# Optimization experiments

Hardware: AMD Instinct MI355X
Metric: run time of the kernel (lower is better)

Reference implementation:

```python
import jax, jax.numpy as jnp
import numpy as np

B, S, E = 2, 2048, 1024
H = 16
HD = E // H           # 64
KD = 64               # k_dim
VD = 64               # v_dim
SCALE = 1.0 / np.float32(np.sqrt(KD))


def setup_inputs() -> dict:
    key = jax.random.key(0)
    ks = jax.random.split(key, 10)
    return {
        "x": jax.random.normal(ks[0], (B, S, E), dtype=jnp.float32),
        "mask": jax.random.uniform(ks[1], (S, S), dtype=jnp.float32),
        "Wq": jax.random.normal(ks[2], (HD, KD), dtype=jnp.float32) * 0.05,
        "bq": jax.random.normal(ks[3], (KD,), dtype=jnp.float32) * 0.05,
        "Wk": jax.random.normal(ks[4], (HD, KD), dtype=jnp.float32) * 0.05,
        "bk": jax.random.normal(ks[5], (KD,), dtype=jnp.float32) * 0.05,
        "Wv": jax.random.normal(ks[6], (HD, VD), dtype=jnp.float32) * 0.05,
        "bv": jax.random.normal(ks[7], (VD,), dtype=jnp.float32) * 0.05,
        "Wo": jax.random.normal(ks[8], (H * VD, E), dtype=jnp.float32) * 0.05,
        "bo": jax.random.normal(ks[9], (E,), dtype=jnp.float32) * 0.05,
    }


def reference(x, mask, Wq, bq, Wk, bk, Wv, bv, Wo, bo):
    b, s, e = x.shape
    # (B, S, E) -> (B, H, S, head_dim)
    xh = x.reshape(b, s, H, HD).transpose(0, 2, 1, 3)
    q = jnp.einsum('bhsd,dk->bhsk', xh, Wq) + bq   # (B,H,S,KD)
    k = jnp.einsum('bhsd,dk->bhsk', xh, Wk) + bk   # (B,H,S,KD)
    v = jnp.einsum('bhsd,dv->bhsv', xh, Wv) + bv   # (B,H,S,VD)
    sim = jnp.einsum('bhqk,bhsk->bhqs', q, k) * SCALE  # (B,H,S,S)
    sim = sim * mask[None, None, :, :]                  # multiplicative mask
    attn = jax.nn.softmax(sim, axis=-1)
    out = jnp.einsum('bhqs,bhsv->bhqv', attn, v)        # (B,H,S,VD)
    out = out.transpose(0, 2, 1, 3).reshape(b, s, H * VD)
    return out @ Wo + bo
```

## Files before the change

### kernel.cpp

```cpp
#include <hip/hip_runtime.h>
#include <hip/hip_bf16.h>

#define SS 2048
#define EE 1024
#define SCALE 0.125f
#define LOG2E 1.44269504088896f

typedef __attribute__((ext_vector_type(8))) short short8;
typedef __attribute__((ext_vector_type(4))) float float4v;
typedef __attribute__((ext_vector_type(8))) unsigned short ushort8;

__device__ __forceinline__ float bf2f(unsigned short u) {
  unsigned int v = ((unsigned int)u) << 16;
  return __uint_as_float(v);
}
__device__ __forceinline__ unsigned short f2bf(float f) {
  unsigned int u = __float_as_uint(f);
  unsigned int lsb = (u >> 16) & 1u;
  u += 0x7fffu + lsb;
  return (unsigned short)(u >> 16);
}
__device__ __forceinline__ unsigned int pk2bf(float a, float b) {
  __hip_bfloat162 h = __float22bfloat162_rn(float2{a, b});
  return *reinterpret_cast<unsigned int*>(&h);
}

__global__ __launch_bounds__(256) void w3t_prep(
    const float* __restrict__ Wq, const float* __restrict__ Wk,
    const float* __restrict__ Wv, unsigned short* __restrict__ W3T)
{
  __shared__ unsigned short t[64 * 65];
  const float* W = (blockIdx.x == 0) ? Wq : (blockIdx.x == 1 ? Wk : Wv);
  int tid = threadIdx.x;
#pragma unroll
  for (int i = 0; i < 16; ++i) {
    int e = tid + i * 256; int d = e >> 6, n = e & 63;
    t[n * 65 + d] = f2bf(W[e]);
  }
  __syncthreads();
  unsigned short* dst = W3T + blockIdx.x * 4096;
#pragma unroll
  for (int i = 0; i < 16; ++i) {
    int e = tid + i * 256; int n = e >> 6, d = e & 63;
    dst[n * 64 + d] = t[n * 65 + d];
  }
}

__global__ __launch_bounds__(256) void qkv_kernel(
    const float* __restrict__ x, const unsigned short* __restrict__ W3T,
    const float* __restrict__ bq, const float* __restrict__ bk,
    const float* __restrict__ bv,
    unsigned short* __restrict__ Q, unsigned short* __restrict__ K,
    unsigned short* __restrict__ Vp)
{
  __shared__ __align__(16) unsigned short w3t[192 * 72];
  __shared__ __align__(16) unsigned short xt[64 * 72];
  __shared__ float sBias[192];
  int tid = threadIdx.x;
  int bh = blockIdx.x >> 5;
  int s0blk = (blockIdx.x & 31) * 64;
  int b = bh >> 4, h = bh & 15;

#pragma unroll
  for (int i = 0; i < 6; ++i) {
    int slot = tid + i * 256;
    int row = slot >> 3, c = slot & 7;
    *(short8*)(w3t + row * 72 + c * 8) = *(const short8*)(W3T + slot * 8);
  }
  if (tid < 192) sBias[tid] = (tid < 64) ? bq[tid] : (tid < 128 ? bk[tid - 64] : bv[tid - 128]);

  const float* xbase = x + ((size_t)(b * SS + s0blk)) * EE + h * 64;
#pragma unroll
  for (int it = 0; it < 4; ++it) {
    int flat = tid + it * 256;
    int row = flat >> 4, ch = flat & 15;
    float4 v = *(const float4*)(xbase + (size_t)row * EE + ch * 4);
    uint2 u; u.x = pk2bf(v.x, v.y); u.y = pk2bf(v.z, v.w);
    *(uint2*)(xt + row * 72 + ch * 4) = u;
  }
  __syncthreads();

  int wv = tid >> 6, lane = tid & 63;
  int li = lane & 15, g = lane >> 4;
  int mrow = wv * 16;

  short8 af[2];
#pragma unroll
  for (int ks = 0; ks < 2; ++ks)
    af[ks] = *(const short8*)(xt + (mrow + li) * 72 + ks * 32 + g * 8);

  float4v acc[12];
#pragma unroll
  for (int i = 0; i < 12; ++i) acc[i] = (float4v){0, 0, 0, 0};
#pragma unroll
  for (int ks = 0; ks < 2; ++ks)
#pragma unroll
    for (int nb = 0; nb < 12; ++nb) {
      short8 bfr = *(const short8*)(w3t + (nb * 16 + li) * 72 + ks * 32 + g * 8);
      acc[nb] = __builtin_amdgcn_mfma_f32_16x16x32_bf16(af[ks], bfr, acc[nb], 0, 0, 0);
    }

  int srow0 = s0blk + mrow + g * 4;
#pragma unroll
  for (int nb = 0; nb < 12; ++nb) {
    float bias = sBias[nb * 16 + li];
    int mtx = nb >> 2, sub = nb & 3;
#pragma unroll
    for (int r = 0; r < 4; ++r) {
      unsigned short ob = f2bf(acc[nb][r] + bias);
      int s = srow0 + r;
      if (mtx == 0)      Q[((size_t)bh * SS + s) * 64 + sub * 16 + li] = ob;
      else if (mtx == 1) K[((size_t)bh * SS + s) * 64 + sub * 16 + li] = ob;
      else {
        int sl = s & 31;
        int pos = ((sl & 15) << 1) | (sl >> 4);
        Vp[(size_t)bh * 131072 + (size_t)(s >> 5) * 2048 + (sub * 16 + li) * 32 + pos] = ob;
      }
    }
  }
}

__global__ __launch_bounds__(256) void mask_prep(
    const float* __restrict__ mask, unsigned short* __restrict__ maskP)
{
  int idx = blockIdx.x * 256 + threadIdx.x;
  int lane = idx & 63, t = (idx >> 6) & 63, qt = idx >> 12;
  int li = lane & 15, g = lane >> 4;
  const float c = SCALE * LOG2E;
  ushort8 o;
#pragma unroll
  for (int sb = 0; sb < 2; ++sb)
#pragma unroll
    for (int r = 0; r < 4; ++r)
      o[sb * 4 + r] = f2bf(mask[(size_t)(qt * 16 + g * 4 + r) * SS + t * 32 + sb * 16 + li] * c);
  *(ushort8*)(maskP + (size_t)idx * 8) = o;
}

__global__ __launch_bounds__(256) void attn_kernel(
    const unsigned short* __restrict__ Q, const unsigned short* __restrict__ K,
    const unsigned short* __restrict__ Vp, const unsigned short* __restrict__ maskP,
    unsigned short* __restrict__ AO)
{
  __shared__ __align__(16) unsigned short kt[32 * 88];
  __shared__ __align__(16) unsigned short vt[64 * 40];
  __shared__ __align__(16) unsigned short pt[4][2][16 * 40];

  int tid = threadIdx.x, wv = tid >> 6, lane = tid & 63;
  int li = lane & 15, g = lane >> 4;
  int bh = blockIdx.x >> 4;
  int q0 = (blockIdx.x & 15) * 128 + wv * 32;

  const unsigned short* Qb0 = Q + ((size_t)bh * SS + q0 + li) * 64;
  const unsigned short* Qb1 = Q + ((size_t)bh * SS + q0 + 16 + li) * 64;
  short8 qf[2][2];
  qf[0][0] = *(const short8*)(Qb0 + g * 8);
  qf[0][1] = *(const short8*)(Qb0 + 32 + g * 8);
  qf[1][0] = *(const short8*)(Qb1 + g * 8);
  qf[1][1] = *(const short8*)(Qb1 + 32 + g * 8);

  const unsigned short* Kg = K + (size_t)bh * SS * 64 + tid * 8;
  const unsigned short* Vg = Vp + (size_t)bh * 131072 + tid * 8;
  const unsigned short* Mg0 = maskP + (size_t)(q0 >> 4) * 32768 + lane * 8;
  const unsigned short* Mg1 = Mg0 + 32768;

  int kldso = (tid >> 3) * 88 + (tid & 7) * 8;
  int vldso = (tid >> 2) * 40 + (tid & 3) * 8;

  float4v acc[2][4];
#pragma unroll
  for (int t = 0; t < 2; ++t)
#pragma unroll
    for (int nb = 0; nb < 4; ++nb) acc[t][nb] = (float4v){0, 0, 0, 0};
  float den[2][4] = {{0, 0, 0, 0}, {0, 0, 0, 0}};
  unsigned short* ptb[2] = {pt[wv][0], pt[wv][1]};

  short8 kreg = *(const short8*)Kg;
  short8 vreg = *(const short8*)Vg;
  ushort8 mc[2];
  mc[0] = *(const ushort8*)Mg0;
  mc[1] = *(const ushort8*)Mg1;

  for (int step = 0; step < 64; ++step) {
    __syncthreads();
    *(short8*)(kt + kldso) = kreg;
    *(short8*)(vt + vldso) = vreg;
    int ns = (step + 1 < 64) ? step + 1 : 0;
    kreg = *(const short8*)(Kg + (size_t)ns * 2048);
    vreg = *(const short8*)(Vg + (size_t)ns * 2048);
    ushort8 mn0 = *(const ushort8*)(Mg0 + (size_t)ns * 512);
    ushort8 mn1 = *(const ushort8*)(Mg1 + (size_t)ns * 512);
    __syncthreads();

    short8 kf[2][2];
#pragma unroll
    for (int sb = 0; sb < 2; ++sb) {
      kf[sb][0] = *(const short8*)(kt + (sb * 16 + li) * 88 + g * 8);
      kf[sb][1] = *(const short8*)(kt + (sb * 16 + li) * 88 + 32 + g * 8);
    }
#pragma unroll
    for (int t = 0; t < 2; ++t) {
      float4v pa0 = {0, 0, 0, 0}, pa1 = {0, 0, 0, 0};
      pa0 = __builtin_amdgcn_mfma_f32_16x16x32_bf16(qf[t][0], kf[0][0], pa0, 0, 0, 0);
      pa0 = __builtin_amdgcn_mfma_f32_16x16x32_bf16(qf[t][1], kf[0][1], pa0, 0, 0, 0);
      pa1 = __builtin_amdgcn_mfma_f32_16x16x32_bf16(qf[t][0], kf[1][0], pa1, 0, 0, 0);
      pa1 = __builtin_amdgcn_mfma_f32_16x16x32_bf16(qf[t][1], kf[1][1], pa1, 0, 0, 0);
#pragma unroll
      for (int r = 0; r < 4; ++r) {
        float p0 = __builtin_amdgcn_exp2f(pa0[r] * bf2f(mc[t][r]));
        float p1 = __builtin_amdgcn_exp2f(pa1[r] * bf2f(mc[t][4 + r]));
        den[t][r] += p0 + p1;
        *(unsigned int*)(ptb[t] + (g * 4 + r) * 40 + li * 2) = pk2bf(p0, p1);
      }
    }
    asm volatile("s_waitcnt lgkmcnt(0)" ::: "memory");
    short8 pf0 = *(const short8*)(ptb[0] + li * 40 + g * 8);
    short8 pf1 = *(const short8*)(ptb[1] + li * 40 + g * 8);
#pragma unroll
    for (int nb = 0; nb < 4; ++nb) {
      short8 vf = *(const short8*)(vt + (nb * 16 + li) * 40 + g * 8);
      acc[0][nb] = __builtin_amdgcn_mfma_f32_16x16x32_bf16(pf0, vf, acc[0][nb], 0, 0, 0);
      acc[1][nb] = __builtin_amdgcn_mfma_f32_16x16x32_bf16(pf1, vf, acc[1][nb], 0, 0, 0);
    }
    mc[0] = mn0; mc[1] = mn1;
  }

#pragma unroll
  for (int t = 0; t < 2; ++t)
#pragma unroll
    for (int r = 0; r < 4; ++r) {
      den[t][r] += __shfl_xor(den[t][r], 1, 64);
      den[t][r] += __shfl_xor(den[t][r], 2, 64);
      den[t][r] += __shfl_xor(den[t][r], 4, 64);
      den[t][r] += __shfl_xor(den[t][r], 8, 64);
    }

  int b = bh >> 4, h = bh & 15;
#pragma unroll
  for (int t = 0; t < 2; ++t)
#pragma unroll
    for (int nb = 0; nb < 4; ++nb)
#pragma unroll
      for (int r = 0; r < 4; ++r) {
        float o = acc[t][nb][r] / den[t][r];
        int s = q0 + t * 16 + g * 4 + r;
        AO[((size_t)(b * SS + s)) * EE + h * 64 + nb * 16 + li] = f2bf(o);
      }
}

__global__ __launch_bounds__(256) void transpose_wo(
    const float* __restrict__ Wo, unsigned short* __restrict__ WoT)
{
  __shared__ unsigned short t[64 * 65];
  int tid = threadIdx.x;
  int k0 = (blockIdx.x >> 4) * 64;
  int n0 = (blockIdx.x & 15) * 64;
#pragma unroll
  for (int i = 0; i < 16; ++i) {
    int idx = tid + i * 256;
    int k = idx >> 6, n = idx & 63;
    t[n * 65 + k] = f2bf(Wo[(size_t)(k0 + k) * 1024 + n0 + n]);
  }
  __syncthreads();
#pragma unroll
  for (int i = 0; i < 16; ++i) {
    int idx = tid + i * 256;
    int n = idx >> 6, k = idx & 63;
    WoT[(size_t)(n0 + n) * 1024 + k0 + k] = t[n * 65 + k];
  }
}

__global__ __launch_bounds__(256) void out_gemm(
    const unsigned short* __restrict__ AO, const unsigned short* __restrict__ WoT,
    const float* __restrict__ bo, float* __restrict__ out)
{
  __shared__ __align__(16) unsigned short at[128 * 72];
  __shared__ __align__(16) unsigned short btl[128 * 72];
  int tid = threadIdx.x, wv = tid >> 6, lane = tid & 63;
  int li = lane & 15, g = lane >> 4;
  int m0 = (blockIdx.x >> 3) * 128;
  int n0 = (blockIdx.x & 7) * 128;
  int wm = (wv & 1) * 64, wn = (wv >> 1) * 64;

  const unsigned short* Ag = AO + (size_t)m0 * 1024;
  const unsigned short* Bg = WoT + (size_t)n0 * 1024;

  short8 apre[4], bpre[4];
  int srow = tid >> 3, scol = (tid & 7) * 8;

  auto ldst = [&](int k0) {
#pragma unroll
    for (int i = 0; i < 4; ++i) {
      apre[i] = *(const short8*)(Ag + (size_t)(srow + i * 32) * 1024 + k0 + scol);
      bpre[i] = *(const short8*)(Bg + (size_t)(srow + i * 32) * 1024 + k0 + scol);
    }
  };

  float4v acc[4][4];
#pragma unroll
  for (int mt = 0; mt < 4; ++mt)
#pragma unroll
    for (int nt = 0; nt < 4; ++nt) acc[mt][nt] = (float4v){0, 0, 0, 0};

  ldst(0);
  for (int k0 = 0; k0 < 1024; k0 += 64) {
    __syncthreads();
#pragma unroll
    for (int i = 0; i < 4; ++i) {
      *(short8*)(at + (srow + i * 32) * 72 + scol) = apre[i];
      *(short8*)(btl + (srow + i * 32) * 72 + scol) = bpre[i];
    }
    int nk = (k0 + 64 < 1024) ? k0 + 64 : 0;
    ldst(nk);
    __syncthreads();
#pragma unroll
    for (int ks = 0; ks < 2; ++ks) {
      short8 afr[4], bfr[4];
#pragma unroll
      for (int mt = 0; mt < 4; ++mt)
        afr[mt] = *(const short8*)(at + (wm + mt * 16 + li) * 72 + ks * 32 + g * 8);
#pragma unroll
      for (int nt = 0; nt < 4; ++nt)
        bfr[nt] = *(const short8*)(btl + (wn + nt * 16 + li) * 72 + ks * 32 + g * 8);
#pragma unroll
      for (int mt = 0; mt < 4; ++mt)
#pragma unroll
        for (int nt = 0; nt < 4; ++nt)
          acc[mt][nt] = __builtin_amdgcn_mfma_f32_16x16x32_bf16(afr[mt], bfr[nt], acc[mt][nt], 0, 0, 0);
    }
  }
#pragma unroll
  for (int nt = 0; nt < 4; ++nt) {
    float bof = bo[n0 + wn + nt * 16 + li];
#pragma unroll
    for (int mt = 0; mt < 4; ++mt)
#pragma unroll
      for (int r = 0; r < 4; ++r)
        out[(size_t)(m0 + wm + mt * 16 + g * 4 + r) * 1024 + n0 + wn + nt * 16 + li] =
            acc[mt][nt][r] + bof;
  }
}

extern "C" void kernel_launch(void* const* d_in, const int* in_sizes, int n_in,
                              void* d_out, int out_size, void* d_ws, size_t ws_size,
                              hipStream_t stream) {
  const float* x    = (const float*)d_in[0];
  const float* mask = (const float*)d_in[1];
  const float* Wq   = (const float*)d_in[2];
  const float* bq   = (const float*)d_in[3];
  const float* Wk   = (const float*)d_in[4];
  const float* bk   = (const float*)d_in[5];
  const float* Wv   = (const float*)d_in[6];
  const float* bv   = (const float*)d_in[7];
  const float* Wo   = (const float*)d_in[8];
  const float* bo   = (const float*)d_in[9];
  float* out = (float*)d_out;

  unsigned short* ws = (unsigned short*)d_ws;
  unsigned short* Q     = ws;
  unsigned short* K     = ws + 4194304;
  unsigned short* Vp    = ws + 8388608;
  unsigned short* AO    = ws + 12582912;
  unsigned short* maskP = ws + 16777216;
  unsigned short* W3T = AO;
  unsigned short* WoT = maskP;

  w3t_prep<<<3, 256, 0, stream>>>(Wq, Wk, Wv, W3T);
  qkv_kernel<<<1024, 256, 0, stream>>>(x, W3T, bq, bk, bv, Q, K, Vp);
  mask_prep<<<2048, 256, 0, stream>>>(mask, maskP);
  attn_kernel<<<512, 256, 0, stream>>>(Q, K, Vp, maskP, AO);
  transpose_wo<<<256, 256, 0, stream>>>(Wo, WoT);
  out_gemm<<<256, 256, 0, stream>>>(AO, WoT, bo, out);
}
```

Before: 202.6 us.

## Keep P in registers, double-buffer K/V, coalesce stores, retile QKV and out GEMM

The attention kernel now computes the transposed score tile (K·Qᵀ) so the exponentiated probabilities land directly in the MFMA operand layout. This drops the per-step LDS round trip for P, and V's permuted layout is changed to match. K/V tiles are double-buffered in LDS with one barrier per step instead of two. The output is staged through LDS for coalesced 16-byte AO stores. Separately, mask_prep is rewritten to use float4 coalesced reads, qkv_kernel processes two 64-row halves per block, and out_gemm uses 128x64 tiles with twice as many blocks. These changes trade LDS traffic and barriers for more register pressure and a mask layout whose indexing must stay consistent.

```diff
diff --git a/kernel.cpp b/kernel.cpp
--- a/kernel.cpp
+++ b/kernel.cpp
@@ -9,6 +9,7 @@
 typedef __attribute__((ext_vector_type(8))) short short8;
 typedef __attribute__((ext_vector_type(4))) float float4v;
 typedef __attribute__((ext_vector_type(8))) unsigned short ushort8;
+typedef __attribute__((ext_vector_type(4))) unsigned int uint4v;
 
 __device__ __forceinline__ float bf2f(unsigned short u) {
   unsigned int v = ((unsigned int)u) << 16;
@@ -57,9 +58,11 @@
   __shared__ __align__(16) unsigned short xt[64 * 72];
   __shared__ float sBias[192];
   int tid = threadIdx.x;
-  int bh = blockIdx.x >> 5;
-  int s0blk = (blockIdx.x & 31) * 64;
+  int bh = blockIdx.x >> 4;
+  int s0blk = (blockIdx.x & 15) * 128;
   int b = bh >> 4, h = bh & 15;
+  int wv = tid >> 6, lane = tid & 63;
+  int li = lane & 15, g = lane >> 4;
 
 #pragma unroll
   for (int i = 0; i < 6; ++i) {
@@ -69,52 +72,53 @@
   }
   if (tid < 192) sBias[tid] = (tid < 64) ? bq[tid] : (tid < 128 ? bk[tid - 64] : bv[tid - 128]);
 
-  const float* xbase = x + ((size_t)(b * SS + s0blk)) * EE + h * 64;
-#pragma unroll
-  for (int it = 0; it < 4; ++it) {
-    int flat = tid + it * 256;
-    int row = flat >> 4, ch = flat & 15;
-    float4 v = *(const float4*)(xbase + (size_t)row * EE + ch * 4);
-    uint2 u; u.x = pk2bf(v.x, v.y); u.y = pk2bf(v.z, v.w);
-    *(uint2*)(xt + row * 72 + ch * 4) = u;
-  }
-  __syncthreads();
-
-  int wv = tid >> 6, lane = tid & 63;
-  int li = lane & 15, g = lane >> 4;
-  int mrow = wv * 16;
-
-  short8 af[2];
-#pragma unroll
-  for (int ks = 0; ks < 2; ++ks)
-    af[ks] = *(const short8*)(xt + (mrow + li) * 72 + ks * 32 + g * 8);
-
-  float4v acc[12];
-#pragma unroll
-  for (int i = 0; i < 12; ++i) acc[i] = (float4v){0, 0, 0, 0};
-#pragma unroll
-  for (int ks = 0; ks < 2; ++ks)
+  for (int half = 0; half < 2; ++half) {
+    int s0 = s0blk + half * 64;
+    if (half) __syncthreads();
+    const float* xbase = x + ((size_t)(b * SS + s0)) * EE + h * 64;
+#pragma unroll
+    for (int it = 0; it < 4; ++it) {
+      int flat = tid + it * 256;
+      int row = flat >> 4, ch = flat & 15;
+      float4 v = *(const float4*)(xbase + (size_t)row * EE + ch * 4);
+      uint2 u; u.x = pk2bf(v.x, v.y); u.y = pk2bf(v.z, v.w);
+      *(uint2*)(xt + row * 72 + ch * 4) = u;
+    }
+    __syncthreads();
+
+    int mrow = wv * 16;
+    short8 af[2];
+#pragma unroll
+    for (int ks = 0; ks < 2; ++ks)
+      af[ks] = *(const short8*)(xt + (mrow + li) * 72 + ks * 32 + g * 8);
+
+    float4v acc[12];
+#pragma unroll
+    for (int i = 0; i < 12; ++i) acc[i] = (float4v){0, 0, 0, 0};
+#pragma unroll
+    for (int ks = 0; ks < 2; ++ks)
+#pragma unroll
+      for (int nb = 0; nb < 12; ++nb) {
+        short8 bfr = *(const short8*)(w3t + (nb * 16 + li) * 72 + ks * 32 + g * 8);
+        acc[nb] = __builtin_amdgcn_mfma_f32_16x16x32_bf16(af[ks], bfr, acc[nb], 0, 0, 0);
+      }
+
+    int srow0 = s0 + mrow + g * 4;
 #pragma unroll
     for (int nb = 0; nb < 12; ++nb) {
-      short8 bfr = *(const short8*)(w3t + (nb * 16 + li) * 72 + ks * 32 + g * 8);
-      acc[nb] = __builtin_amdgcn_mfma_f32_16x16x32_bf16(af[ks], bfr, acc[nb], 0, 0, 0);
-    }
-
-  int srow0 = s0blk + mrow + g * 4;
-#pragma unroll
-  for (int nb = 0; nb < 12; ++nb) {
-    float bias = sBias[nb * 16 + li];
-    int mtx = nb >> 2, sub = nb & 3;
-#pragma unroll
-    for (int r = 0; r < 4; ++r) {
-      unsigned short ob = f2bf(acc[nb][r] + bias);
-      int s = srow0 + r;
-      if (mtx == 0)      Q[((size_t)bh * SS + s) * 64 + sub * 16 + li] = ob;
-      else if (mtx == 1) K[((size_t)bh * SS + s) * 64 + sub * 16 + li] = ob;
-      else {
-        int sl = s & 31;
-        int pos = ((sl & 15) << 1) | (sl >> 4);
-        Vp[(size_t)bh * 131072 + (size_t)(s >> 5) * 2048 + (sub * 16 + li) * 32 + pos] = ob;
+      float bias = sBias[nb * 16 + li];
+      int mtx = nb >> 2, sub = nb & 3;
+#pragma unroll
+      for (int r = 0; r < 4; ++r) {
+        unsigned short ob = f2bf(acc[nb][r] + bias);
+        int s = srow0 + r;
+        if (mtx == 0)      Q[((size_t)bh * SS + s) * 64 + sub * 16 + li] = ob;
+        else if (mtx == 1) K[((size_t)bh * SS + s) * 64 + sub * 16 + li] = ob;
+        else {
+          int sl = s & 31;
+          int pos = ((sl >> 2) & 3) * 8 + ((sl >> 4) & 1) * 4 + (sl & 3);
+          Vp[(size_t)bh * 131072 + (size_t)(s >> 5) * 2048 + (sub * 16 + li) * 32 + pos] = ob;
+        }
       }
     }
   }
@@ -124,16 +128,18 @@
     const float* __restrict__ mask, unsigned short* __restrict__ maskP)
 {
   int idx = blockIdx.x * 256 + threadIdx.x;
-  int lane = idx & 63, t = (idx >> 6) & 63, qt = idx >> 12;
+  int lane = idx & 63, step = (idx >> 6) & 63, qt = idx >> 12;
   int li = lane & 15, g = lane >> 4;
   const float c = SCALE * LOG2E;
-  ushort8 o;
-#pragma unroll
-  for (int sb = 0; sb < 2; ++sb)
-#pragma unroll
-    for (int r = 0; r < 4; ++r)
-      o[sb * 4 + r] = f2bf(mask[(size_t)(qt * 16 + g * 4 + r) * SS + t * 32 + sb * 16 + li] * c);
-  *(ushort8*)(maskP + (size_t)idx * 8) = o;
+  const float* mrow = mask + (size_t)(qt * 16 + li) * SS + step * 32 + g * 4;
+  float4 a = *(const float4*)mrow;
+  float4 bb = *(const float4*)(mrow + 16);
+  uint4v o;
+  o.x = pk2bf(a.x * c, a.y * c);
+  o.y = pk2bf(a.z * c, a.w * c);
+  o.z = pk2bf(bb.x * c, bb.y * c);
+  o.w = pk2bf(bb.z * c, bb.w * c);
+  *(uint4v*)(maskP + (size_t)idx * 8) = o;
 }
 
 __global__ __launch_bounds__(256) void attn_kernel(
@@ -141,28 +147,29 @@
     const unsigned short* __restrict__ Vp, const unsigned short* __restrict__ maskP,
     unsigned short* __restrict__ AO)
 {
-  __shared__ __align__(16) unsigned short kt[32 * 88];
-  __shared__ __align__(16) unsigned short vt[64 * 40];
-  __shared__ __align__(16) unsigned short pt[4][2][16 * 40];
+  __shared__ __align__(16) unsigned short lds[2 * 2816 + 2 * 2560];
+  unsigned short* ktb0 = lds;
+  unsigned short* ktb1 = lds + 2816;
+  unsigned short* vtb0 = lds + 5632;
+  unsigned short* vtb1 = lds + 8192;
 
   int tid = threadIdx.x, wv = tid >> 6, lane = tid & 63;
   int li = lane & 15, g = lane >> 4;
   int bh = blockIdx.x >> 4;
   int q0 = (blockIdx.x & 15) * 128 + wv * 32;
 
-  const unsigned short* Qb0 = Q + ((size_t)bh * SS + q0 + li) * 64;
-  const unsigned short* Qb1 = Q + ((size_t)bh * SS + q0 + 16 + li) * 64;
   short8 qf[2][2];
-  qf[0][0] = *(const short8*)(Qb0 + g * 8);
-  qf[0][1] = *(const short8*)(Qb0 + 32 + g * 8);
-  qf[1][0] = *(const short8*)(Qb1 + g * 8);
-  qf[1][1] = *(const short8*)(Qb1 + 32 + g * 8);
+#pragma unroll
+  for (int t = 0; t < 2; ++t) {
+    const unsigned short* Qb = Q + ((size_t)bh * SS + q0 + t * 16 + li) * 64;
+    qf[t][0] = *(const short8*)(Qb + g * 8);
+    qf[t][1] = *(const short8*)(Qb + 32 + g * 8);
+  }
 
   const unsigned short* Kg = K + (size_t)bh * SS * 64 + tid * 8;
   const unsigned short* Vg = Vp + (size_t)bh * 131072 + tid * 8;
   const unsigned short* Mg0 = maskP + (size_t)(q0 >> 4) * 32768 + lane * 8;
   const unsigned short* Mg1 = Mg0 + 32768;
-
   int kldso = (tid >> 3) * 88 + (tid & 7) * 8;
   int vldso = (tid >> 2) * 40 + (tid & 3) * 8;
 
@@ -171,25 +178,27 @@
   for (int t = 0; t < 2; ++t)
 #pragma unroll
     for (int nb = 0; nb < 4; ++nb) acc[t][nb] = (float4v){0, 0, 0, 0};
-  float den[2][4] = {{0, 0, 0, 0}, {0, 0, 0, 0}};
-  unsigned short* ptb[2] = {pt[wv][0], pt[wv][1]};
+  float2 den2[2] = {{0.f, 0.f}, {0.f, 0.f}};
 
   short8 kreg = *(const short8*)Kg;
   short8 vreg = *(const short8*)Vg;
-  ushort8 mc[2];
-  mc[0] = *(const ushort8*)Mg0;
-  mc[1] = *(const ushort8*)Mg1;
+  uint4v mc[2];
+  mc[0] = *(const uint4v*)Mg0;
+  mc[1] = *(const uint4v*)Mg1;
+  *(short8*)(ktb0 + kldso) = kreg;
+  *(short8*)(vtb0 + vldso) = vreg;
+  __syncthreads();
 
   for (int step = 0; step < 64; ++step) {
-    __syncthreads();
-    *(short8*)(kt + kldso) = kreg;
-    *(short8*)(vt + vldso) = vreg;
+    const unsigned short* kt = (step & 1) ? ktb1 : ktb0;
+    const unsigned short* vt = (step & 1) ? vtb1 : vtb0;
+    unsigned short* ktn = (step & 1) ? ktb0 : ktb1;
+    unsigned short* vtn = (step & 1) ? vtb0 : vtb1;
     int ns = (step + 1 < 64) ? step + 1 : 0;
     kreg = *(const short8*)(Kg + (size_t)ns * 2048);
     vreg = *(const short8*)(Vg + (size_t)ns * 2048);
-    ushort8 mn0 = *(const ushort8*)(Mg0 + (size_t)ns * 512);
-    ushort8 mn1 = *(const ushort8*)(Mg1 + (size_t)ns * 512);
-    __syncthreads();
+    uint4v mn0 = *(const uint4v*)(Mg0 + (size_t)ns * 512);
+    uint4v mn1 = *(const uint4v*)(Mg1 + (size_t)ns * 512);
 
     short8 kf[2][2];
 #pragma unroll
@@ -197,54 +206,70 @@
       kf[sb][0] = *(const short8*)(kt + (sb * 16 + li) * 88 + g * 8);
       kf[sb][1] = *(const short8*)(kt + (sb * 16 + li) * 88 + 32 + g * 8);
     }
+
+    uint4v pw[2];
 #pragma unroll
     for (int t = 0; t < 2; ++t) {
-      float4v pa0 = {0, 0, 0, 0}, pa1 = {0, 0, 0, 0};
-      pa0 = __builtin_amdgcn_mfma_f32_16x16x32_bf16(qf[t][0], kf[0][0], pa0, 0, 0, 0);
-      pa0 = __builtin_amdgcn_mfma_f32_16x16x32_bf16(qf[t][1], kf[0][1], pa0, 0, 0, 0);
-      pa1 = __builtin_amdgcn_mfma_f32_16x16x32_bf16(qf[t][0], kf[1][0], pa1, 0, 0, 0);
-      pa1 = __builtin_amdgcn_mfma_f32_16x16x32_bf16(qf[t][1], kf[1][1], pa1, 0, 0, 0);
-#pragma unroll
-      for (int r = 0; r < 4; ++r) {
-        float p0 = __builtin_amdgcn_exp2f(pa0[r] * bf2f(mc[t][r]));
-        float p1 = __builtin_amdgcn_exp2f(pa1[r] * bf2f(mc[t][4 + r]));
-        den[t][r] += p0 + p1;
-        *(unsigned int*)(ptb[t] + (g * 4 + r) * 40 + li * 2) = pk2bf(p0, p1);
+#pragma unroll
+      for (int sb = 0; sb < 2; ++sb) {
+        float4v st = {0, 0, 0, 0};
+        st = __builtin_amdgcn_mfma_f32_16x16x32_bf16(kf[sb][0], qf[t][0], st, 0, 0, 0);
+        st = __builtin_amdgcn_mfma_f32_16x16x32_bf16(kf[sb][1], qf[t][1], st, 0, 0, 0);
+#pragma unroll
+        for (int hh = 0; hh < 2; ++hh) {
+          unsigned int mm = (t == 0) ? mc[0][sb * 2 + hh] : mc[1][sb * 2 + hh];
+          float mlo = __uint_as_float(mm << 16);
+          float mhi = __uint_as_float(mm & 0xffff0000u);
+          float p0 = __builtin_amdgcn_exp2f(st[2 * hh] * mlo);
+          float p1 = __builtin_amdgcn_exp2f(st[2 * hh + 1] * mhi);
+          den2[t].x += p0;
+          den2[t].y += p1;
+          pw[t][sb * 2 + hh] = pk2bf(p0, p1);
+        }
       }
     }
-    asm volatile("s_waitcnt lgkmcnt(0)" ::: "memory");
-    short8 pf0 = *(const short8*)(ptb[0] + li * 40 + g * 8);
-    short8 pf1 = *(const short8*)(ptb[1] + li * 40 + g * 8);
+    short8 pf0 = *(short8*)&pw[0];
+    short8 pf1 = *(short8*)&pw[1];
 #pragma unroll
     for (int nb = 0; nb < 4; ++nb) {
       short8 vf = *(const short8*)(vt + (nb * 16 + li) * 40 + g * 8);
-      acc[0][nb] = __builtin_amdgcn_mfma_f32_16x16x32_bf16(pf0, vf, acc[0][nb], 0, 0, 0);
-      acc[1][nb] = __builtin_amdgcn_mfma_f32_16x16x32_bf16(pf1, vf, acc[1][nb], 0, 0, 0);
-    }
+      acc[0][nb] = __builtin_amdgcn_mfma_f32_16x16x32_bf16(vf, pf0, acc[0][nb], 0, 0, 0);
+      acc[1][nb] = __builtin_amdgcn_mfma_f32_16x16x32_bf16(vf, pf1, acc[1][nb], 0, 0, 0);
+    }
+    *(short8*)(ktn + kldso) = kreg;
+    *(short8*)(vtn + vldso) = vreg;
     mc[0] = mn0; mc[1] = mn1;
-  }
-
+    __syncthreads();
+  }
+
+  float rd[2];
+#pragma unroll
+  for (int t = 0; t < 2; ++t) {
+    float d = den2[t].x + den2[t].y;
+    d += __shfl_xor(d, 16, 64);
+    d += __shfl_xor(d, 32, 64);
+    rd[t] = 1.0f / d;
+  }
+
+  unsigned short* tr = lds + wv * 2304;
 #pragma unroll
   for (int t = 0; t < 2; ++t)
 #pragma unroll
-    for (int r = 0; r < 4; ++r) {
-      den[t][r] += __shfl_xor(den[t][r], 1, 64);
-      den[t][r] += __shfl_xor(den[t][r], 2, 64);
-      den[t][r] += __shfl_xor(den[t][r], 4, 64);
-      den[t][r] += __shfl_xor(den[t][r], 8, 64);
-    }
+    for (int nb = 0; nb < 4; ++nb) {
+      int base = (t * 16 + li) * 72 + nb * 16 + g * 4;
+      *(unsigned int*)(tr + base)     = pk2bf(acc[t][nb][0] * rd[t], acc[t][nb][1] * rd[t]);
+      *(unsigned int*)(tr + base + 2) = pk2bf(acc[t][nb][2] * rd[t], acc[t][nb][3] * rd[t]);
+    }
+  asm volatile("s_waitcnt lgkmcnt(0)" ::: "memory");
 
   int b = bh >> 4, h = bh & 15;
-#pragma unroll
-  for (int t = 0; t < 2; ++t)
-#pragma unroll
-    for (int nb = 0; nb < 4; ++nb)
-#pragma unroll
-      for (int r = 0; r < 4; ++r) {
-        float o = acc[t][nb][r] / den[t][r];
-        int s = q0 + t * 16 + g * 4 + r;
-        AO[((size_t)(b * SS + s)) * EE + h * 64 + nb * 16 + li] = f2bf(o);
-      }
+  int rrow = lane >> 3, part = lane & 7;
+#pragma unroll
+  for (int i = 0; i < 4; ++i) {
+    int row = i * 8 + rrow;
+    short8 ov = *(const short8*)(tr + row * 72 + part * 8);
+    *(short8*)(AO + ((size_t)(b * SS + q0 + row)) * EE + h * 64 + part * 8) = ov;
+  }
 }
 
 __global__ __launch_bounds__(256) void transpose_wo(
@@ -274,62 +299,63 @@
     const float* __restrict__ bo, float* __restrict__ out)
 {
   __shared__ __align__(16) unsigned short at[128 * 72];
-  __shared__ __align__(16) unsigned short btl[128 * 72];
+  __shared__ __align__(16) unsigned short bt[64 * 72];
   int tid = threadIdx.x, wv = tid >> 6, lane = tid & 63;
   int li = lane & 15, g = lane >> 4;
-  int m0 = (blockIdx.x >> 3) * 128;
-  int n0 = (blockIdx.x & 7) * 128;
-  int wm = (wv & 1) * 64, wn = (wv >> 1) * 64;
+  int m0 = (blockIdx.x >> 4) * 128;
+  int n0 = (blockIdx.x & 15) * 64;
+  int wm = (wv & 1) * 64, wn = (wv >> 1) * 32;
 
   const unsigned short* Ag = AO + (size_t)m0 * 1024;
   const unsigned short* Bg = WoT + (size_t)n0 * 1024;
-
-  short8 apre[4], bpre[4];
   int srow = tid >> 3, scol = (tid & 7) * 8;
 
+  short8 apre[4], bpre[2];
   auto ldst = [&](int k0) {
 #pragma unroll
-    for (int i = 0; i < 4; ++i) {
+    for (int i = 0; i < 4; ++i)
       apre[i] = *(const short8*)(Ag + (size_t)(srow + i * 32) * 1024 + k0 + scol);
+#pragma unroll
+    for (int i = 0; i < 2; ++i)
       bpre[i] = *(const short8*)(Bg + (size_t)(srow + i * 32) * 1024 + k0 + scol);
-    }
   };
 
-  float4v acc[4][4];
+  float4v acc[4][2];
 #pragma unroll
   for (int mt = 0; mt < 4; ++mt)
 #pragma unroll
-    for (int nt = 0; nt < 4; ++nt) acc[mt][nt] = (float4v){0, 0, 0, 0};
+    for (int nt = 0; nt < 2; ++nt) acc[mt][nt] = (float4v){0, 0, 0, 0};
 
   ldst(0);
   for (int k0 = 0; k0 < 1024; k0 += 64) {
     __syncthreads();
 #pragma unroll
-    for (int i = 0; i < 4; ++i) {
+    for (int i = 0; i < 4; ++i)
       *(short8*)(at + (srow + i * 32) * 72 + scol) = apre[i];
-      *(short8*)(btl + (srow + i * 32) * 72 + scol) = bpre[i];
-    }
+#pragma unroll
+    for (int i = 0; i < 2; ++i)
+      *(short8*)(bt + (srow + i * 32) * 72 + scol) = bpre[i];
     int nk = (k0 + 64 < 1024) ? k0 + 64 : 0;
     ldst(nk);
     __syncthreads();
 #pragma unroll
     for (int ks = 0; ks < 2; ++ks) {
-      short8 afr[4], bfr[4];
+      short8 afr[4], bfr[2];
 #pragma unroll
       for (int mt = 0; mt < 4; ++mt)
         afr[mt] = *(const short8*)(at + (wm + mt * 16 + li) * 72 + ks * 32 + g * 8);
 #pragma unroll
-      for (int nt = 0; nt < 4; ++nt)
-        bfr[nt] = *(const short8*)(btl + (wn + nt * 16 + li) * 72 + ks * 32 + g * 8);
+      for (int nt = 0; nt < 2; ++nt)
+        bfr[nt] = *(const short8*)(bt + (wn + nt * 16 + li) * 72 + ks * 32 + g * 8);
 #pragma unroll
       for (int mt = 0; mt < 4; ++mt)
 #pragma unroll
-        for (int nt = 0; nt < 4; ++nt)
+        for (int nt = 0; nt < 2; ++nt)
           acc[mt][nt] = __builtin_amdgcn_mfma_f32_16x16x32_bf16(afr[mt], bfr[nt], acc[mt][nt], 0, 0, 0);
     }
   }
 #pragma unroll
-  for (int nt = 0; nt < 4; ++nt) {
+  for (int nt = 0; nt < 2; ++nt) {
     float bof = bo[n0 + wn + nt * 16 + li];
 #pragma unroll
     for (int mt = 0; mt < 4; ++mt)
@@ -365,9 +391,9 @@
   unsigned short* WoT = maskP;
 
   w3t_prep<<<3, 256, 0, stream>>>(Wq, Wk, Wv, W3T);
-  qkv_kernel<<<1024, 256, 0, stream>>>(x, W3T, bq, bk, bv, Q, K, Vp);
+  qkv_kernel<<<512, 256, 0, stream>>>(x, W3T, bq, bk, bv, Q, K, Vp);
   mask_prep<<<2048, 256, 0, stream>>>(mask, maskP);
   attn_kernel<<<512, 256, 0, stream>>>(Q, K, Vp, maskP, AO);
   transpose_wo<<<256, 256, 0, stream>>>(Wo, WoT);
-  out_gemm<<<256, 256, 0, stream>>>(AO, WoT, bo, out);
-}
+  out_gemm<<<512, 256, 0, stream>>>(AO, WoT, bo, out);
+}
```

Result: faster. 188.7 us (-6.9%).
